# Optimization experiments

Measured on AMD Instinct MI355X. Metric: run time of the kernel, lower is better.

The kernel has to match this reference:

```python
import jax, jax.numpy as jnp
import numpy as np

B, S, D, H, FF, L = 32, 512, 512, 16, 2048, 3
DH = D // H
EPS = 1e-3


def setup_inputs() -> dict:
    key = jax.random.key(0)
    ks = jax.random.split(key, 8)
    sc = 0.02
    n = lambda k, shp: (jax.random.normal(k, shp, jnp.float32) * sc)
    return {
        "input_seq": jax.random.normal(ks[0], (B, S, D), jnp.float32),
        "Wq": n(ks[1], (L, D, D)), "bq": jnp.zeros((L, D), jnp.float32),
        "Wk": n(ks[2], (L, D, D)), "bk": jnp.zeros((L, D), jnp.float32),
        "Wv": n(ks[3], (L, D, D)), "bv": jnp.zeros((L, D), jnp.float32),
        "g1": jnp.ones((L, D), jnp.float32), "be1": jnp.zeros((L, D), jnp.float32),
        "W1": n(ks[4], (L, D, FF)), "b1": jnp.zeros((L, FF), jnp.float32),
        "W2": n(ks[5], (L, FF, D)), "b2": jnp.zeros((L, D), jnp.float32),
        "g2": jnp.ones((L, D), jnp.float32), "be2": jnp.zeros((L, D), jnp.float32),
    }


def batch_norm(x, g, b):
    # training-mode BatchNorm1d over channels=last dim; stats over (batch, seq)
    m = jnp.mean(x, axis=(0, 1))
    v = jnp.var(x, axis=(0, 1))  # biased, as torch BN uses for normalization
    return (x - m) * jax.lax.rsqrt(v + EPS) * g + b


def encoder_fwd(x, Wq, bq, Wk, bk, Wv, bv, g1, be1, W1, b1, W2, b2, g2, be2):
    scale = 1.0 / jnp.sqrt(jnp.float32(DH))
    for i in range(L):
        # --- multi-head attention block ---
        q = jax.nn.relu(x @ Wq[i] + bq[i]).reshape(B, S, H, DH)
        k = jax.nn.relu(x @ Wk[i] + bk[i]).reshape(B, S, H, DH)
        v = jax.nn.relu(x @ Wv[i] + bv[i]).reshape(B, S, H, DH)
        scores = jnp.einsum("bshd,bthd->bhst", q, k) * scale
        attn = jax.nn.softmax(scores, axis=-1)  # dropout = identity (eval)
        o = jnp.einsum("bhst,bthd->bshd", attn, v).reshape(B, S, D)
        x = batch_norm(o + x, g1[i], be1[i])
        # --- feed-forward block ---
        h = jax.nn.relu(x @ W1[i] + b1[i])
        x = batch_norm(h @ W2[i] + b2[i] + x, g2[i], be2[i])
    return x


def reference(input_seq, Wq, bq, Wk, bk, Wv, bv, g1, be1, W1, b1, W2, b2, g2, be2):
    return encoder_fwd(input_seq, Wq, bq, Wk, bk, Wv, bv, g1, be1, W1, b1, W2, b2, g2, be2)
```

## Files before the change

kernel.cpp:

```cpp
#include <hip/hip_runtime.h>
#include <hip/hip_bf16.h>

typedef __bf16 bf16;
typedef __bf16 bf16x2 __attribute__((ext_vector_type(2)));
typedef __bf16 bf16x4 __attribute__((ext_vector_type(4)));
typedef __bf16 bf16x8 __attribute__((ext_vector_type(8)));
typedef float f32x4 __attribute__((ext_vector_type(4)));

#define SEQ 512
#define DIM 512
#define NH 16
#define DH 32
#define FFD 2048
#define NBATCH 32
#define MTOT (NBATCH * SEQ)

__device__ __forceinline__ void gl_lds16(const bf16* g, bf16* l) {
  __builtin_amdgcn_global_load_lds(
      (const __attribute__((address_space(1))) void*)g,
      (__attribute__((address_space(3))) void*)l, 16, 0, 0);
}

template <int EPI>
__global__ __launch_bounds__(256, 2)
void gemm_bt(const bf16* __restrict__ A, const bf16* __restrict__ BT,
             const float* __restrict__ bias, bf16* __restrict__ out,
             int N, int K) {
  __shared__ bf16 As[128 * 32];
  __shared__ bf16 Bs[128 * 32];
  const int tid = threadIdx.x;
  const int lane = tid & 63, wave = tid >> 6;
  const int wr = wave >> 1, wc = wave & 1;
  const int lo = lane & 15, hi = lane >> 4;
  const int m0 = blockIdx.y * 128, n0 = blockIdx.x * 128;
  const bf16* Ab = A + (size_t)m0 * K;
  const bf16* Bb = BT + (size_t)n0 * K;
  f32x4 acc[4][4] = {};
  for (int k0 = 0; k0 < K; k0 += 32) {
    __syncthreads();
    {
      const int i0 = tid, i1 = tid + 256;
      gl_lds16(Ab + (size_t)(i0 >> 2) * K + k0 + (i0 & 3) * 8, As + i0 * 8);
      gl_lds16(Ab + (size_t)(i1 >> 2) * K + k0 + (i1 & 3) * 8, As + i1 * 8);
      gl_lds16(Bb + (size_t)(i0 >> 2) * K + k0 + (i0 & 3) * 8, Bs + i0 * 8);
      gl_lds16(Bb + (size_t)(i1 >> 2) * K + k0 + (i1 & 3) * 8, Bs + i1 * 8);
    }
    __syncthreads();
    bf16x8 a[4], b[4];
#pragma unroll
    for (int i = 0; i < 4; ++i) {
      a[i] = *(const bf16x8*)(As + (wr * 64 + i * 16 + lo) * 32 + hi * 8);
      b[i] = *(const bf16x8*)(Bs + (wc * 64 + i * 16 + lo) * 32 + hi * 8);
    }
#pragma unroll
    for (int i = 0; i < 4; ++i)
#pragma unroll
      for (int j = 0; j < 4; ++j)
        acc[i][j] = __builtin_amdgcn_mfma_f32_16x16x32_bf16(a[i], b[j], acc[i][j], 0, 0, 0);
  }
#pragma unroll
  for (int i = 0; i < 4; ++i) {
#pragma unroll
    for (int j = 0; j < 4; ++j) {
      const int n = n0 + wc * 64 + j * 16 + lo;
      const float bs = bias[n];
#pragma unroll
      for (int r = 0; r < 4; ++r) {
        const int m = m0 + wr * 64 + i * 16 + hi * 4 + r;
        float v = acc[i][j][r] + bs;
        if (EPI != 2) v = fmaxf(v, 0.f);
        if (EPI == 0) {
          const int b_ = m >> 9, s_ = m & 511, h_ = n >> 5, dh_ = n & 31;
          out[(((size_t)(b_ * NH + h_)) * SEQ + s_) * DH + dh_] = (bf16)v;
        } else {
          out[(size_t)m * N + n] = (bf16)v;
        }
      }
    }
  }
}

__global__ __launch_bounds__(256, 2)
void attn_kernel(const bf16* __restrict__ Qb, const bf16* __restrict__ Kb,
                 const bf16* __restrict__ Vb, bf16* __restrict__ O) {
  __shared__ bf16 Vt[32][520];
  __shared__ bf16 P[4][16][40];
  const int bh = blockIdx.x;
  const int tid = threadIdx.x, lane = tid & 63, wave = tid >> 6;
  const int lo = lane & 15, hi = lane >> 4;
  const bf16* Qp = Qb + (size_t)bh * SEQ * DH;
  const bf16* Kp = Kb + (size_t)bh * SEQ * DH;
  const bf16* Vp = Vb + (size_t)bh * SEQ * DH;
  for (int r = tid; r < SEQ; r += 256) {
    bf16x8 v0 = *(const bf16x8*)(Vp + r * DH);
    bf16x8 v1 = *(const bf16x8*)(Vp + r * DH + 8);
    bf16x8 v2 = *(const bf16x8*)(Vp + r * DH + 16);
    bf16x8 v3 = *(const bf16x8*)(Vp + r * DH + 24);
#pragma unroll
    for (int c = 0; c < 8; ++c) {
      Vt[c][r] = v0[c]; Vt[8 + c][r] = v1[c];
      Vt[16 + c][r] = v2[c]; Vt[24 + c][r] = v3[c];
    }
  }
  __syncthreads();
  const float CEXP = 0.17677669529663687f * 1.44269504088896f;
  const int b_ = bh >> 4, h_ = bh & 15;
  for (int chunk = wave; chunk < 32; chunk += 4) {
    const int s0 = chunk * 16;
    bf16x8 qf = *(const bf16x8*)(Qp + (s0 + lo) * DH + hi * 8);
    f32x4 acc[32];
#pragma unroll
    for (int t = 0; t < 32; ++t) {
      bf16x8 kf = *(const bf16x8*)(Kp + (t * 16 + lo) * DH + hi * 8);
      acc[t] = __builtin_amdgcn_mfma_f32_16x16x32_bf16(qf, kf, (f32x4){0.f, 0.f, 0.f, 0.f}, 0, 0, 0);
    }
    float mx[4], sm[4], inv[4];
#pragma unroll
    for (int j = 0; j < 4; ++j) mx[j] = acc[0][j];
#pragma unroll
    for (int t = 1; t < 32; ++t)
#pragma unroll
      for (int j = 0; j < 4; ++j) mx[j] = fmaxf(mx[j], acc[t][j]);
#pragma unroll
    for (int d = 1; d < 16; d <<= 1)
#pragma unroll
      for (int j = 0; j < 4; ++j) mx[j] = fmaxf(mx[j], __shfl_xor(mx[j], d));
#pragma unroll
    for (int j = 0; j < 4; ++j) sm[j] = 0.f;
#pragma unroll
    for (int t = 0; t < 32; ++t)
#pragma unroll
      for (int j = 0; j < 4; ++j) {
        float p = __builtin_amdgcn_exp2f((acc[t][j] - mx[j]) * CEXP);
        acc[t][j] = p; sm[j] += p;
      }
#pragma unroll
    for (int d = 1; d < 16; d <<= 1)
#pragma unroll
      for (int j = 0; j < 4; ++j) sm[j] += __shfl_xor(sm[j], d);
#pragma unroll
    for (int j = 0; j < 4; ++j) inv[j] = 1.f / sm[j];
    f32x4 o0 = {0.f, 0.f, 0.f, 0.f}, o1 = {0.f, 0.f, 0.f, 0.f};
#pragma unroll
    for (int kk = 0; kk < 16; ++kk) {
#pragma unroll
      for (int tt = 0; tt < 2; ++tt)
#pragma unroll
        for (int j = 0; j < 4; ++j)
          P[wave][hi * 4 + j][tt * 16 + lo] = (bf16)acc[kk * 2 + tt][j];
      bf16x8 pa  = *(const bf16x8*)&P[wave][lo][hi * 8];
      bf16x8 vf0 = *(const bf16x8*)&Vt[lo][kk * 32 + hi * 8];
      bf16x8 vf1 = *(const bf16x8*)&Vt[16 + lo][kk * 32 + hi * 8];
      o0 = __builtin_amdgcn_mfma_f32_16x16x32_bf16(pa, vf0, o0, 0, 0, 0);
      o1 = __builtin_amdgcn_mfma_f32_16x16x32_bf16(pa, vf1, o1, 0, 0, 0);
    }
#pragma unroll
    for (int j = 0; j < 4; ++j) {
      const int s_ = s0 + hi * 4 + j;
      const size_t base = ((size_t)(b_ * SEQ + s_)) * DIM + h_ * DH;
      O[base + lo]      = (bf16)(o0[j] * inv[j]);
      O[base + 16 + lo] = (bf16)(o1[j] * inv[j]);
    }
  }
}

__global__ __launch_bounds__(256)
void cast_kernel(const float* __restrict__ in, bf16* __restrict__ out) {
  const size_t i = ((size_t)blockIdx.x * 256 + threadIdx.x) * 4;
  const float4 v = *(const float4*)(in + i);
  bf16x4 o;
  o[0] = (bf16)v.x; o[1] = (bf16)v.y; o[2] = (bf16)v.z; o[3] = (bf16)v.w;
  *(bf16x4*)(out + i) = o;
}

__global__ __launch_bounds__(256)
void transpose_cast(const float* __restrict__ W, bf16* __restrict__ WT, int K, int N) {
  __shared__ float t[32][33];
  const int l = blockIdx.z;
  const float* Wl = W + (size_t)l * K * N;
  bf16* WTl = WT + (size_t)l * K * N;
  const int n0 = blockIdx.x * 32, k0 = blockIdx.y * 32;
  const int tx = threadIdx.x, ty = threadIdx.y;
#pragma unroll
  for (int r = 0; r < 32; r += 8)
    t[ty + r][tx] = Wl[(size_t)(k0 + ty + r) * N + n0 + tx];
  __syncthreads();
#pragma unroll
  for (int r = 0; r < 32; r += 8)
    WTl[(size_t)(n0 + ty + r) * K + k0 + tx] = (bf16)t[tx][ty + r];
}

__global__ __launch_bounds__(256)
void bn_stats(const bf16* __restrict__ o, const float* __restrict__ x,
              float* __restrict__ part) {
  const int blk = blockIdx.x, tid = threadIdx.x;
  const int c = tid * 2;
  const size_t base = (size_t)blk * 64 * DIM + c;
  float s0 = 0, s1 = 0, q0 = 0, q1 = 0;
  for (int r = 0; r < 64; ++r) {
    const size_t idx = base + (size_t)r * DIM;
    const float2 xv = *(const float2*)(x + idx);
    const bf16x2 ov = *(const bf16x2*)(o + idx);
    const float a = xv.x + (float)ov[0];
    const float b = xv.y + (float)ov[1];
    s0 += a; q0 += a * a; s1 += b; q1 += b * b;
  }
  float4 w = {s0, q0, s1, q1};
  *(float4*)(part + ((size_t)blk * DIM + c) * 2) = w;
}

__global__ __launch_bounds__(256)
void bn_finalize(const float* __restrict__ part, const float* __restrict__ g,
                 const float* __restrict__ be, float* __restrict__ coef) {
  const int c = blockIdx.x * 256 + threadIdx.x;
  float s = 0, q = 0;
  for (int b = 0; b < 256; ++b) {
    const float2 p = *(const float2*)(part + ((size_t)b * DIM + c) * 2);
    s += p.x; q += p.y;
  }
  const float inv_n = 1.f / (float)MTOT;
  const float mean = s * inv_n;
  const float var = q * inv_n - mean * mean;
  const float k = g[c] * rsqrtf(var + 1e-3f);
  coef[c] = k;
  coef[DIM + c] = be[c] - mean * k;
}

__global__ __launch_bounds__(256)
void bn_apply(const bf16* __restrict__ o, const float* __restrict__ x,
              const float* __restrict__ coef, float* __restrict__ xout,
              bf16* __restrict__ xbout) {
  const size_t i = ((size_t)blockIdx.x * 256 + threadIdx.x) * 4;
  const int c = (int)(i & (DIM - 1));
  const float4 xv = *(const float4*)(x + i);
  const bf16x2 o01 = *(const bf16x2*)(o + i);
  const bf16x2 o23 = *(const bf16x2*)(o + i + 2);
  const float y0 = (xv.x + (float)o01[0]) * coef[c]     + coef[DIM + c];
  const float y1 = (xv.y + (float)o01[1]) * coef[c + 1] + coef[DIM + c + 1];
  const float y2 = (xv.z + (float)o23[0]) * coef[c + 2] + coef[DIM + c + 2];
  const float y3 = (xv.w + (float)o23[1]) * coef[c + 3] + coef[DIM + c + 3];
  float4 yo = {y0, y1, y2, y3};
  *(float4*)(xout + i) = yo;
  if (xbout) {
    bf16x4 yb;
    yb[0] = (bf16)y0; yb[1] = (bf16)y1; yb[2] = (bf16)y2; yb[3] = (bf16)y3;
    *(bf16x4*)(xbout + i) = yb;
  }
}

#define OFF_XB   ((size_t)0)
#define OFF_Q    ((size_t)16777216)
#define OFF_K    ((size_t)33554432)
#define OFF_V    ((size_t)50331648)
#define OFF_O    ((size_t)67108864)
#define OFF_H    ((size_t)16777216)
#define OFF_Z    ((size_t)83886080)
#define OFF_X    ((size_t)100663296)
#define OFF_WQT  ((size_t)134217728)
#define OFF_WKT  ((size_t)135790592)
#define OFF_WVT  ((size_t)137363456)
#define OFF_W1T  ((size_t)138936320)
#define OFF_W2T  ((size_t)145227776)
#define OFF_PART ((size_t)151519232)
#define OFF_COEF ((size_t)152567808)

extern "C" void kernel_launch(void* const* d_in, const int* in_sizes, int n_in,
                              void* d_out, int out_size, void* d_ws, size_t ws_size,
                              hipStream_t stream) {
  const float* x_in = (const float*)d_in[0];
  const float* Wq = (const float*)d_in[1];
  const float* bq = (const float*)d_in[2];
  const float* Wk = (const float*)d_in[3];
  const float* bk = (const float*)d_in[4];
  const float* Wv = (const float*)d_in[5];
  const float* bv = (const float*)d_in[6];
  const float* g1 = (const float*)d_in[7];
  const float* be1 = (const float*)d_in[8];
  const float* W1 = (const float*)d_in[9];
  const float* b1 = (const float*)d_in[10];
  const float* W2 = (const float*)d_in[11];
  const float* b2 = (const float*)d_in[12];
  const float* g2 = (const float*)d_in[13];
  const float* be2 = (const float*)d_in[14];
  float* out = (float*)d_out;

  char* ws = (char*)d_ws;
  bf16* xb   = (bf16*)(ws + OFF_XB);
  bf16* qb   = (bf16*)(ws + OFF_Q);
  bf16* kb   = (bf16*)(ws + OFF_K);
  bf16* vb   = (bf16*)(ws + OFF_V);
  bf16* ob   = (bf16*)(ws + OFF_O);
  bf16* hb   = (bf16*)(ws + OFF_H);
  bf16* zb   = (bf16*)(ws + OFF_Z);
  float* xf  = (float*)(ws + OFF_X);
  bf16* wqT  = (bf16*)(ws + OFF_WQT);
  bf16* wkT  = (bf16*)(ws + OFF_WKT);
  bf16* wvT  = (bf16*)(ws + OFF_WVT);
  bf16* w1T  = (bf16*)(ws + OFF_W1T);
  bf16* w2T  = (bf16*)(ws + OFF_W2T);
  float* part = (float*)(ws + OFF_PART);
  float* coef = (float*)(ws + OFF_COEF);

  const dim3 blk32(32, 8);
  transpose_cast<<<dim3(16, 16, 3), blk32, 0, stream>>>(Wq, wqT, 512, 512);
  transpose_cast<<<dim3(16, 16, 3), blk32, 0, stream>>>(Wk, wkT, 512, 512);
  transpose_cast<<<dim3(16, 16, 3), blk32, 0, stream>>>(Wv, wvT, 512, 512);
  transpose_cast<<<dim3(64, 16, 3), blk32, 0, stream>>>(W1, w1T, 512, 2048);
  transpose_cast<<<dim3(16, 64, 3), blk32, 0, stream>>>(W2, w2T, 2048, 512);
  cast_kernel<<<8192, 256, 0, stream>>>(x_in, xb);

  for (int l = 0; l < 3; ++l) {
    const float* xcur = (l == 0) ? x_in : xf;
    gemm_bt<0><<<dim3(4, 128), 256, 0, stream>>>(xb, wqT + (size_t)l * 512 * 512, bq + l * 512, qb, 512, 512);
    gemm_bt<0><<<dim3(4, 128), 256, 0, stream>>>(xb, wkT + (size_t)l * 512 * 512, bk + l * 512, kb, 512, 512);
    gemm_bt<0><<<dim3(4, 128), 256, 0, stream>>>(xb, wvT + (size_t)l * 512 * 512, bv + l * 512, vb, 512, 512);
    attn_kernel<<<512, 256, 0, stream>>>(qb, kb, vb, ob);
    bn_stats<<<256, 256, 0, stream>>>(ob, xcur, part);
    bn_finalize<<<2, 256, 0, stream>>>(part, g1 + l * 512, be1 + l * 512, coef);
    bn_apply<<<8192, 256, 0, stream>>>(ob, xcur, coef, xf, xb);
    gemm_bt<1><<<dim3(16, 128), 256, 0, stream>>>(xb, w1T + (size_t)l * 2048 * 512, b1 + l * 2048, hb, 2048, 512);
    gemm_bt<2><<<dim3(4, 128), 256, 0, stream>>>(hb, w2T + (size_t)l * 512 * 2048, b2 + l * 512, zb, 512, 2048);
    bn_stats<<<256, 256, 0, stream>>>(zb, xf, part);
    bn_finalize<<<2, 256, 0, stream>>>(part, g2 + l * 512, be2 + l * 512, coef);
    if (l < 2)
      bn_apply<<<8192, 256, 0, stream>>>(zb, xf, coef, xf, xb);
    else
      bn_apply<<<8192, 256, 0, stream>>>(zb, xf, coef, out, (bf16*)nullptr);
  }
}
```

Before: 1.012 ms.

## Keep residual in bf16, pre-transpose V in GEMM epilogue, drop softmax max pass

The residual stream is now kept only in bf16, so the separate fp32 copy is gone and the batch-norm stats and apply kernels read and write half the bytes. The apply kernel is also vectorised to 8 elements per thread. The V projection GEMM gains an epilogue that writes V already transposed, so the attention kernel reads it straight from global memory instead of staging a transposed copy in LDS. Attention is split into two query halves per (batch, head), launched at higher occupancy, and computes softmax in one pass without subtracting the row max. That last shortcut depends on the scores staying small enough not to overflow exp, and bf16 residuals lower the precision of the carried activations.

```diff
diff --git a/kernel.cpp b/kernel.cpp
--- a/kernel.cpp
+++ b/kernel.cpp
@@ -64,102 +64,93 @@
     for (int j = 0; j < 4; ++j) {
       const int n = n0 + wc * 64 + j * 16 + lo;
       const float bs = bias[n];
+      float v[4];
 #pragma unroll
       for (int r = 0; r < 4; ++r) {
-        const int m = m0 + wr * 64 + i * 16 + hi * 4 + r;
-        float v = acc[i][j][r] + bs;
-        if (EPI != 2) v = fmaxf(v, 0.f);
-        if (EPI == 0) {
+        v[r] = acc[i][j][r] + bs;
+        if (EPI != 2) v[r] = fmaxf(v[r], 0.f);
+      }
+      const int mb = m0 + wr * 64 + i * 16 + hi * 4;
+      if (EPI == 0) {
+#pragma unroll
+        for (int r = 0; r < 4; ++r) {
+          const int m = mb + r;
           const int b_ = m >> 9, s_ = m & 511, h_ = n >> 5, dh_ = n & 31;
-          out[(((size_t)(b_ * NH + h_)) * SEQ + s_) * DH + dh_] = (bf16)v;
-        } else {
-          out[(size_t)m * N + n] = (bf16)v;
+          out[(((size_t)(b_ * NH + h_)) * SEQ + s_) * DH + dh_] = (bf16)v[r];
         }
+      } else if (EPI == 3) {
+        const int b_ = mb >> 9, s_ = mb & 511, h_ = n >> 5, dh_ = n & 31;
+        bf16x4 vv;
+#pragma unroll
+        for (int r = 0; r < 4; ++r) vv[r] = (bf16)v[r];
+        *(bf16x4*)&out[(((size_t)(b_ * NH + h_)) * DH + dh_) * SEQ + s_] = vv;
+      } else {
+#pragma unroll
+        for (int r = 0; r < 4; ++r)
+          out[(size_t)(mb + r) * N + n] = (bf16)v[r];
       }
     }
   }
 }
 
-__global__ __launch_bounds__(256, 2)
+__global__ __launch_bounds__(256, 4)
 void attn_kernel(const bf16* __restrict__ Qb, const bf16* __restrict__ Kb,
-                 const bf16* __restrict__ Vb, bf16* __restrict__ O) {
-  __shared__ bf16 Vt[32][520];
-  __shared__ bf16 P[4][16][40];
-  const int bh = blockIdx.x;
+                 const bf16* __restrict__ Vt, bf16* __restrict__ O) {
+  __shared__ bf16 P[4][16][264];
+  const int half = blockIdx.x, bh = blockIdx.y;
   const int tid = threadIdx.x, lane = tid & 63, wave = tid >> 6;
   const int lo = lane & 15, hi = lane >> 4;
   const bf16* Qp = Qb + (size_t)bh * SEQ * DH;
   const bf16* Kp = Kb + (size_t)bh * SEQ * DH;
-  const bf16* Vp = Vb + (size_t)bh * SEQ * DH;
-  for (int r = tid; r < SEQ; r += 256) {
-    bf16x8 v0 = *(const bf16x8*)(Vp + r * DH);
-    bf16x8 v1 = *(const bf16x8*)(Vp + r * DH + 8);
-    bf16x8 v2 = *(const bf16x8*)(Vp + r * DH + 16);
-    bf16x8 v3 = *(const bf16x8*)(Vp + r * DH + 24);
-#pragma unroll
-    for (int c = 0; c < 8; ++c) {
-      Vt[c][r] = v0[c]; Vt[8 + c][r] = v1[c];
-      Vt[16 + c][r] = v2[c]; Vt[24 + c][r] = v3[c];
-    }
-  }
-  __syncthreads();
+  const bf16* Vp = Vt + (size_t)bh * DH * SEQ;
   const float CEXP = 0.17677669529663687f * 1.44269504088896f;
   const int b_ = bh >> 4, h_ = bh & 15;
-  for (int chunk = wave; chunk < 32; chunk += 4) {
-    const int s0 = chunk * 16;
-    bf16x8 qf = *(const bf16x8*)(Qp + (s0 + lo) * DH + hi * 8);
-    f32x4 acc[32];
-#pragma unroll
-    for (int t = 0; t < 32; ++t) {
-      bf16x8 kf = *(const bf16x8*)(Kp + (t * 16 + lo) * DH + hi * 8);
-      acc[t] = __builtin_amdgcn_mfma_f32_16x16x32_bf16(qf, kf, (f32x4){0.f, 0.f, 0.f, 0.f}, 0, 0, 0);
-    }
-    float mx[4], sm[4], inv[4];
-#pragma unroll
-    for (int j = 0; j < 4; ++j) mx[j] = acc[0][j];
-#pragma unroll
-    for (int t = 1; t < 32; ++t)
-#pragma unroll
-      for (int j = 0; j < 4; ++j) mx[j] = fmaxf(mx[j], acc[t][j]);
+  for (int c = wave; c < 16; c += 4) {
+    const int s0 = half * 256 + c * 16;
+    const bf16x8 qf = *(const bf16x8*)(Qp + (s0 + lo) * DH + hi * 8);
+    float sm[4] = {0.f, 0.f, 0.f, 0.f};
+    f32x4 o0 = {0.f, 0.f, 0.f, 0.f}, o1 = {0.f, 0.f, 0.f, 0.f};
+#pragma unroll
+    for (int h2 = 0; h2 < 2; ++h2) {
+      f32x4 acc[16];
+#pragma unroll
+      for (int t = 0; t < 16; ++t) {
+        const bf16x8 kf = *(const bf16x8*)(Kp + (h2 * 256 + t * 16 + lo) * DH + hi * 8);
+        acc[t] = __builtin_amdgcn_mfma_f32_16x16x32_bf16(qf, kf, (f32x4){0.f, 0.f, 0.f, 0.f}, 0, 0, 0);
+      }
+#pragma unroll
+      for (int t = 0; t < 16; ++t)
+#pragma unroll
+        for (int j = 0; j < 4; ++j) {
+          const float p = __builtin_amdgcn_exp2f(acc[t][j] * CEXP);
+          acc[t][j] = p; sm[j] += p;
+        }
+#pragma unroll
+      for (int t = 0; t < 16; ++t)
+#pragma unroll
+        for (int j = 0; j < 4; ++j)
+          P[wave][hi * 4 + j][t * 16 + lo] = (bf16)acc[t][j];
+#pragma unroll
+      for (int kkl = 0; kkl < 8; ++kkl) {
+        const bf16x8 pa = *(const bf16x8*)&P[wave][lo][kkl * 32 + hi * 8];
+        const int kg = h2 * 256 + kkl * 32 + hi * 8;
+        const bf16x8 vf0 = *(const bf16x8*)(Vp + (size_t)lo * SEQ + kg);
+        const bf16x8 vf1 = *(const bf16x8*)(Vp + (size_t)(16 + lo) * SEQ + kg);
+        o0 = __builtin_amdgcn_mfma_f32_16x16x32_bf16(pa, vf0, o0, 0, 0, 0);
+        o1 = __builtin_amdgcn_mfma_f32_16x16x32_bf16(pa, vf1, o1, 0, 0, 0);
+      }
+    }
 #pragma unroll
     for (int d = 1; d < 16; d <<= 1)
 #pragma unroll
-      for (int j = 0; j < 4; ++j) mx[j] = fmaxf(mx[j], __shfl_xor(mx[j], d));
-#pragma unroll
-    for (int j = 0; j < 4; ++j) sm[j] = 0.f;
-#pragma unroll
-    for (int t = 0; t < 32; ++t)
-#pragma unroll
-      for (int j = 0; j < 4; ++j) {
-        float p = __builtin_amdgcn_exp2f((acc[t][j] - mx[j]) * CEXP);
-        acc[t][j] = p; sm[j] += p;
-      }
-#pragma unroll
-    for (int d = 1; d < 16; d <<= 1)
-#pragma unroll
       for (int j = 0; j < 4; ++j) sm[j] += __shfl_xor(sm[j], d);
 #pragma unroll
-    for (int j = 0; j < 4; ++j) inv[j] = 1.f / sm[j];
-    f32x4 o0 = {0.f, 0.f, 0.f, 0.f}, o1 = {0.f, 0.f, 0.f, 0.f};
-#pragma unroll
-    for (int kk = 0; kk < 16; ++kk) {
-#pragma unroll
-      for (int tt = 0; tt < 2; ++tt)
-#pragma unroll
-        for (int j = 0; j < 4; ++j)
-          P[wave][hi * 4 + j][tt * 16 + lo] = (bf16)acc[kk * 2 + tt][j];
-      bf16x8 pa  = *(const bf16x8*)&P[wave][lo][hi * 8];
-      bf16x8 vf0 = *(const bf16x8*)&Vt[lo][kk * 32 + hi * 8];
-      bf16x8 vf1 = *(const bf16x8*)&Vt[16 + lo][kk * 32 + hi * 8];
-      o0 = __builtin_amdgcn_mfma_f32_16x16x32_bf16(pa, vf0, o0, 0, 0, 0);
-      o1 = __builtin_amdgcn_mfma_f32_16x16x32_bf16(pa, vf1, o1, 0, 0, 0);
-    }
-#pragma unroll
     for (int j = 0; j < 4; ++j) {
+      const float inv = 1.f / sm[j];
       const int s_ = s0 + hi * 4 + j;
       const size_t base = ((size_t)(b_ * SEQ + s_)) * DIM + h_ * DH;
-      O[base + lo]      = (bf16)(o0[j] * inv[j]);
-      O[base + 16 + lo] = (bf16)(o1[j] * inv[j]);
+      O[base + lo]      = (bf16)(o0[j] * inv);
+      O[base + 16 + lo] = (bf16)(o1[j] * inv);
     }
   }
 }
@@ -191,7 +182,7 @@
 }
 
 __global__ __launch_bounds__(256)
-void bn_stats(const bf16* __restrict__ o, const float* __restrict__ x,
+void bn_stats(const bf16* __restrict__ o, const bf16* __restrict__ x,
               float* __restrict__ part) {
   const int blk = blockIdx.x, tid = threadIdx.x;
   const int c = tid * 2;
@@ -199,10 +190,10 @@
   float s0 = 0, s1 = 0, q0 = 0, q1 = 0;
   for (int r = 0; r < 64; ++r) {
     const size_t idx = base + (size_t)r * DIM;
-    const float2 xv = *(const float2*)(x + idx);
+    const bf16x2 xv = *(const bf16x2*)(x + idx);
     const bf16x2 ov = *(const bf16x2*)(o + idx);
-    const float a = xv.x + (float)ov[0];
-    const float b = xv.y + (float)ov[1];
+    const float a = (float)xv[0] + (float)ov[0];
+    const float b = (float)xv[1] + (float)ov[1];
     s0 += a; q0 += a * a; s1 += b; q1 += b * b;
   }
   float4 w = {s0, q0, s1, q1};
@@ -227,24 +218,27 @@
 }
 
 __global__ __launch_bounds__(256)
-void bn_apply(const bf16* __restrict__ o, const float* __restrict__ x,
-              const float* __restrict__ coef, float* __restrict__ xout,
-              bf16* __restrict__ xbout) {
-  const size_t i = ((size_t)blockIdx.x * 256 + threadIdx.x) * 4;
+void bn_apply(const bf16* __restrict__ o, const bf16* __restrict__ x,
+              const float* __restrict__ coef, bf16* __restrict__ xout,
+              float* __restrict__ fout) {
+  const size_t i = ((size_t)blockIdx.x * 256 + threadIdx.x) * 8;
   const int c = (int)(i & (DIM - 1));
-  const float4 xv = *(const float4*)(x + i);
-  const bf16x2 o01 = *(const bf16x2*)(o + i);
-  const bf16x2 o23 = *(const bf16x2*)(o + i + 2);
-  const float y0 = (xv.x + (float)o01[0]) * coef[c]     + coef[DIM + c];
-  const float y1 = (xv.y + (float)o01[1]) * coef[c + 1] + coef[DIM + c + 1];
-  const float y2 = (xv.z + (float)o23[0]) * coef[c + 2] + coef[DIM + c + 2];
-  const float y3 = (xv.w + (float)o23[1]) * coef[c + 3] + coef[DIM + c + 3];
-  float4 yo = {y0, y1, y2, y3};
-  *(float4*)(xout + i) = yo;
-  if (xbout) {
-    bf16x4 yb;
-    yb[0] = (bf16)y0; yb[1] = (bf16)y1; yb[2] = (bf16)y2; yb[3] = (bf16)y3;
-    *(bf16x4*)(xbout + i) = yb;
+  const bf16x8 ov = *(const bf16x8*)(o + i);
+  const bf16x8 xv = *(const bf16x8*)(x + i);
+  float y[8];
+#pragma unroll
+  for (int j = 0; j < 8; ++j)
+    y[j] = ((float)ov[j] + (float)xv[j]) * coef[c + j] + coef[DIM + c + j];
+  if (fout) {
+    float4 a = {y[0], y[1], y[2], y[3]};
+    float4 b = {y[4], y[5], y[6], y[7]};
+    *(float4*)(fout + i) = a;
+    *(float4*)(fout + i + 4) = b;
+  } else {
+    bf16x8 yb;
+#pragma unroll
+    for (int j = 0; j < 8; ++j) yb[j] = (bf16)y[j];
+    *(bf16x8*)(xout + i) = yb;
   }
 }
 
@@ -255,14 +249,13 @@
 #define OFF_O    ((size_t)67108864)
 #define OFF_H    ((size_t)16777216)
 #define OFF_Z    ((size_t)83886080)
-#define OFF_X    ((size_t)100663296)
-#define OFF_WQT  ((size_t)134217728)
-#define OFF_WKT  ((size_t)135790592)
-#define OFF_WVT  ((size_t)137363456)
-#define OFF_W1T  ((size_t)138936320)
-#define OFF_W2T  ((size_t)145227776)
-#define OFF_PART ((size_t)151519232)
-#define OFF_COEF ((size_t)152567808)
+#define OFF_WQT  ((size_t)100663296)
+#define OFF_WKT  ((size_t)102236160)
+#define OFF_WVT  ((size_t)103809024)
+#define OFF_W1T  ((size_t)105381888)
+#define OFF_W2T  ((size_t)111673344)
+#define OFF_PART ((size_t)117964800)
+#define OFF_COEF ((size_t)119013376)
 
 extern "C" void kernel_launch(void* const* d_in, const int* in_sizes, int n_in,
                               void* d_out, int out_size, void* d_ws, size_t ws_size,
@@ -292,7 +285,6 @@
   bf16* ob   = (bf16*)(ws + OFF_O);
   bf16* hb   = (bf16*)(ws + OFF_H);
   bf16* zb   = (bf16*)(ws + OFF_Z);
-  float* xf  = (float*)(ws + OFF_X);
   bf16* wqT  = (bf16*)(ws + OFF_WQT);
   bf16* wkT  = (bf16*)(ws + OFF_WKT);
   bf16* wvT  = (bf16*)(ws + OFF_WVT);
@@ -310,21 +302,20 @@
   cast_kernel<<<8192, 256, 0, stream>>>(x_in, xb);
 
   for (int l = 0; l < 3; ++l) {
-    const float* xcur = (l == 0) ? x_in : xf;
     gemm_bt<0><<<dim3(4, 128), 256, 0, stream>>>(xb, wqT + (size_t)l * 512 * 512, bq + l * 512, qb, 512, 512);
     gemm_bt<0><<<dim3(4, 128), 256, 0, stream>>>(xb, wkT + (size_t)l * 512 * 512, bk + l * 512, kb, 512, 512);
-    gemm_bt<0><<<dim3(4, 128), 256, 0, stream>>>(xb, wvT + (size_t)l * 512 * 512, bv + l * 512, vb, 512, 512);
-    attn_kernel<<<512, 256, 0, stream>>>(qb, kb, vb, ob);
-    bn_stats<<<256, 256, 0, stream>>>(ob, xcur, part);
+    gemm_bt<3><<<dim3(4, 128), 256, 0, stream>>>(xb, wvT + (size_t)l * 512 * 512, bv + l * 512, vb, 512, 512);
+    attn_kernel<<<dim3(2, 512), 256, 0, stream>>>(qb, kb, vb, ob);
+    bn_stats<<<256, 256, 0, stream>>>(ob, xb, part);
     bn_finalize<<<2, 256, 0, stream>>>(part, g1 + l * 512, be1 + l * 512, coef);
-    bn_apply<<<8192, 256, 0, stream>>>(ob, xcur, coef, xf, xb);
+    bn_apply<<<4096, 256, 0, stream>>>(ob, xb, coef, xb, nullptr);
     gemm_bt<1><<<dim3(16, 128), 256, 0, stream>>>(xb, w1T + (size_t)l * 2048 * 512, b1 + l * 2048, hb, 2048, 512);
     gemm_bt<2><<<dim3(4, 128), 256, 0, stream>>>(hb, w2T + (size_t)l * 512 * 2048, b2 + l * 512, zb, 512, 2048);
-    bn_stats<<<256, 256, 0, stream>>>(zb, xf, part);
+    bn_stats<<<256, 256, 0, stream>>>(zb, xb, part);
     bn_finalize<<<2, 256, 0, stream>>>(part, g2 + l * 512, be2 + l * 512, coef);
     if (l < 2)
-      bn_apply<<<8192, 256, 0, stream>>>(zb, xf, coef, xf, xb);
+      bn_apply<<<4096, 256, 0, stream>>>(zb, xb, coef, xb, nullptr);
     else
-      bn_apply<<<8192, 256, 0, stream>>>(zb, xf, coef, out, (bf16*)nullptr);
-  }
-}
+      bn_apply<<<4096, 256, 0, stream>>>(zb, xb, coef, nullptr, out);
+  }
+}
```

After: 1.545 ms. 52.6% more time.
